# Performance work log

Hardware: AMD Instinct MI355X
Metric: run time of the kernel (lower is better)

## Reference

```python
import jax, jax.numpy as jnp
import numpy as np

BATCH = 4096
DIM = 128
TEMP = 0.5

def setup_inputs() -> dict:
    key = jax.random.key(0)
    k1, k2 = jax.random.split(key)
    proj_1 = jax.random.normal(k1, (BATCH, DIM), dtype=jnp.float32)
    proj_2 = jax.random.normal(k2, (BATCH, DIM), dtype=jnp.float32)
    return {"proj_1": proj_1, "proj_2": proj_2}

def _l2norm(x, eps=1e-12):
    # matches F.normalize(p=2, dim=1)
    n = jnp.sqrt(jnp.sum(x * x, axis=1, keepdims=True))
    return x / jnp.maximum(n, eps)

def reference(proj_1, proj_2):
    B = proj_1.shape[0]
    z_i = _l2norm(proj_1)
    z_j = _l2norm(proj_2)
    reps = jnp.concatenate([z_i, z_j], axis=0)          # [2B, D]
    # cosine similarity of normalized vectors == dot product; (2B,D)x(D,2B) matmul
    sim = reps @ reps.T                                 # [2B, 2B]
    sim_ij = jnp.einsum('bd,bd->b', z_i, z_j)           # diag(sim, +B)
    sim_ji = sim_ij                                     # diag(sim, -B) is symmetric
    positives = jnp.concatenate([sim_ij, sim_ji], axis=0)  # [2B]
    nominator = jnp.exp(positives / TEMP)
    mask = (~jnp.eye(2 * B, dtype=bool)).astype(sim.dtype)
    denominator = jnp.sum(mask * jnp.exp(sim / TEMP), axis=1)  # [2B]
    all_losses = -jnp.log(nominator / denominator)
    loss = jnp.sum(all_losses) / (2 * B)
    return loss
```

## Files before the change

### kernel.cpp

```cpp
#include <hip/hip_runtime.h>
#include <math.h>

#define BATCH 4096
#define DIM 128
#define TWO_B 8192
#define SCALE 1.69864374f
#define NBLK 1024
#define MAGIC 0x6D2F9A3Bu

typedef float floatx4 __attribute__((ext_vector_type(4)));
typedef int   intx4  __attribute__((ext_vector_type(4)));
typedef long  longx2 __attribute__((ext_vector_type(2)));

__device__ __forceinline__ longx2 as_l2(intx4 v) {
    union { intx4 a; longx2 b; } u; u.a = v; return u.b;
}
__device__ __forceinline__ unsigned char to_fp8(float v) {
    return (unsigned char)(__builtin_amdgcn_cvt_pk_fp8_f32(v, v, 0, false) & 0xff);
}
template <typename T>
__device__ __forceinline__ void st_agent(T* p, T v) {
    __hip_atomic_store(p, v, __ATOMIC_RELAXED, __HIP_MEMORY_SCOPE_AGENT);
}
template <typename T>
__device__ __forceinline__ T ld_agent(const T* p) {
    return __hip_atomic_load(p, __ATOMIC_RELAXED, __HIP_MEMORY_SCOPE_AGENT);
}


__global__ __launch_bounds__(256, 4) void fused_kernel(const float* __restrict__ p1,
                                                       const float* __restrict__ p2,
                                                       unsigned char* __restrict__ repsF,
                                                       float* __restrict__ pos,
                                                       float* __restrict__ denom,
                                                       unsigned int* __restrict__ gsync,
                                                       float* __restrict__ out) {
    __shared__ float lds[4][16][68];
    __shared__ float red[4];
    int tid = threadIdx.x;
    int wid = tid >> 6, lane = tid & 63;
    int bid = blockIdx.x;
    unsigned int* arr  = gsync;
    unsigned int* done = gsync + NBLK;
    unsigned int* go   = gsync + 2 * NBLK;

    if (tid < 8) st_agent(&denom[bid * 8 + tid], 0.0f);
    {
        int b = bid * 4 + wid;
        const float* r1 = p1 + (size_t)b * DIM;
        const float* r2 = p2 + (size_t)b * DIM;
        float x0 = r1[lane], x1 = r1[lane + 64];
        float y0 = r2[lane], y1 = r2[lane + 64];
        float s1 = x0 * x0 + x1 * x1;
        float s2 = y0 * y0 + y1 * y1;
        float s12 = x0 * y0 + x1 * y1;
        #pragma unroll
        for (int off = 32; off; off >>= 1) {
            s1  += __shfl_xor(s1, off);
            s2  += __shfl_xor(s2, off);
            s12 += __shfl_xor(s12, off);
        }
        float n1 = fmaxf(sqrtf(s1), 1e-12f);
        float n2 = fmaxf(sqrtf(s2), 1e-12f);
        float i1 = SCALE / n1;
        float i2 = SCALE / n2;

        int r1i = b, r2i = b + BATCH;
        int off0 = ((lane >> 5) & 1) * 8 + ((lane >> 3) & 3) * 256 + (lane & 7);
        size_t a1 = (size_t)(r1i >> 4) * 2048 + (r1i & 15) * 16 + off0;
        size_t a2 = (size_t)(r2i >> 4) * 2048 + (r2i & 15) * 16 + off0;
        st_agent(&repsF[a1],        to_fp8(x0 * i1));
        st_agent(&repsF[a1 + 1024], to_fp8(x1 * i1));
        st_agent(&repsF[a2],        to_fp8(y0 * i2));
        st_agent(&repsF[a2 + 1024], to_fp8(y1 * i2));

        if (lane == 0) st_agent(&pos[b], s12 / (n1 * n2));
    }

    __syncthreads();
    if (tid == 0) {
        asm volatile("s_waitcnt vmcnt(0)" ::: "memory");
        st_agent(&arr[bid], MAGIC);
    }
    if (bid == 0 && wid == 0) {
        int guard = 0;
        for (;;) {
            int ok = 1;
            #pragma unroll
            for (int j = 0; j < 16; ++j)
                ok &= (ld_agent(&arr[lane + j * 64]) == MAGIC) ? 1 : 0;
            if (__all(ok) || ++guard > (1 << 20)) break;
            __builtin_amdgcn_s_sleep(2);
        }
        if (lane == 0) {
            asm volatile("s_waitcnt vmcnt(0)" ::: "memory");
            st_agent(go, MAGIC);
        }
    }
    if (tid == 0) {
        int guard = 0;
        while (ld_agent(go) != MAGIC && ++guard < (1 << 20))
            __builtin_amdgcn_s_sleep(2);
    }
    __syncthreads();
    asm volatile("" ::: "memory");

    {
        int wm = wid >> 1, wn = wid & 1;
        int lr = lane & 15, q = lane >> 4;
        const char* base = (const char*)repsF;
        int lofs = q * 256 + lr * 16;

        for (int t = bid; t < 65 * 32; t += NBLK) {
            int r = t / 65;
            int c = t - r * 65;
            int TM, TN;
            if (c < 64 - r) { TM = r;      TN = r + c; }
            else            { TM = 63 - r; TN = TM + (c - (64 - r)); }
            if (TM == TN && wm == 1 && wn == 0) continue;
            int tm = 2 * TM + wm, tn = 2 * TN + wn;
            bool diag = (tm == tn);

            const char* ab = base + tm * 8192 + lofs;
            const char* bb = base + tn * 8192 + lofs;

            longx2 aF[4][2], bF[4][2];
            #pragma unroll
            for (int mi = 0; mi < 4; ++mi)
                #pragma unroll
                for (int h = 0; h < 2; ++h) {
                    aF[mi][h] = as_l2(*(const intx4*)(ab + mi * 2048 + h * 1024));
                    bF[mi][h] = as_l2(*(const intx4*)(bb + mi * 2048 + h * 1024));
                }

            float cs[4] = {0.0f, 0.0f, 0.0f, 0.0f};
            floatx4 rpacc[4];

            #pragma unroll
            for (int p = 0; p < 2; ++p) {
                floatx4 acc[4][2] = {};
                #pragma unroll
                for (int ck = 0; ck < 4; ++ck) {
                    int h = ck >> 1, sel = ck & 1;
                    #pragma unroll
                    for (int mi = 0; mi < 4; ++mi)
                        #pragma unroll
                        for (int nn = 0; nn < 2; ++nn)
                            acc[mi][nn] = __builtin_amdgcn_mfma_f32_16x16x32_fp8_fp8(
                                aF[mi][h][sel], bF[2 * p + nn][h][sel], acc[mi][nn], 0, 0, 0);
                }
                #pragma unroll
                for (int mi = 0; mi < 4; ++mi) {
                    #pragma unroll
                    for (int reg = 0; reg < 4; ++reg) {
                        float e0 = __builtin_amdgcn_exp2f(acc[mi][0][reg]);
                        float e1 = __builtin_amdgcn_exp2f(acc[mi][1][reg]);
                        if (diag && (q * 4 + reg) == lr) {
                            if (mi == 2 * p)     e0 = 0.0f;
                            if (mi == 2 * p + 1) e1 = 0.0f;
                        }
                        cs[2 * p]     += e0;
                        cs[2 * p + 1] += e1;
                        float rsum = e0 + e1;
                        rpacc[mi][reg] = (p == 0) ? rsum : (rpacc[mi][reg] + rsum);
                    }
                }
            }

            float* myl = &lds[wid][0][0];
            #pragma unroll
            for (int mi = 0; mi < 4; ++mi)
                *(floatx4*)&myl[lr * 68 + mi * 16 + q * 4] = rpacc[mi];
            asm volatile("s_waitcnt lgkmcnt(0)" ::: "memory");
            {
                float rs = 0.0f;
                #pragma unroll
                for (int j = 0; j < 16; ++j)
                    rs += myl[j * 68 + lane];
                atomicAdd(&denom[tm * 64 + lane], rs);
            }
            if (!diag) {
                #pragma unroll
                for (int ni = 0; ni < 4; ++ni) {
                    cs[ni] += __shfl_xor(cs[ni], 16);
                    cs[ni] += __shfl_xor(cs[ni], 32);
                }
                if (q == 0) {
                    #pragma unroll
                    for (int ni = 0; ni < 4; ++ni)
                        atomicAdd(&denom[tn * 64 + ni * 16 + lr], cs[ni]);
                }
            }
        }
    }

    __syncthreads();
    if (tid == 0) {
        asm volatile("s_waitcnt vmcnt(0)" ::: "memory");
        st_agent(&done[bid], MAGIC);
    }
    if (bid != 0) return;
    if (wid == 0) {
        int guard = 0;
        for (;;) {
            int ok = 1;
            #pragma unroll
            for (int j = 0; j < 16; ++j)
                ok &= (ld_agent(&done[lane + j * 64]) == MAGIC) ? 1 : 0;
            if (__all(ok) || ++guard > (1 << 20)) break;
            __builtin_amdgcn_s_sleep(2);
        }
    }
    __syncthreads();
    asm volatile("" ::: "memory");

    {
        float v = 0.0f;
        #pragma unroll
        for (int k = 0; k < 32; ++k) {
            int rr = k * 256 + tid;
            v += __logf(ld_agent(&denom[rr])) - 2.0f * ld_agent(&pos[rr & (BATCH - 1)]);
        }
        #pragma unroll
        for (int off = 32; off; off >>= 1) v += __shfl_xor(v, off);
        if (lane == 0) red[wid] = v;
        __syncthreads();
        if (tid == 0)
            out[0] = ((red[0] + red[1]) + (red[2] + red[3])) * (1.0f / TWO_B);
    }
}

extern "C" void kernel_launch(void* const* d_in, const int* in_sizes, int n_in,
                              void* d_out, int out_size, void* d_ws, size_t ws_size,
                              hipStream_t stream) {
    const float* p1 = (const float*)d_in[0];
    const float* p2 = (const float*)d_in[1];
    float* out = (float*)d_out;

    char* ws = (char*)d_ws;
    unsigned char* repsF = (unsigned char*)ws;
    float* pos   = (float*)(ws + (size_t)TWO_B * DIM);
    float* denom = pos + BATCH;
    unsigned int* gsync = (unsigned int*)(denom + TWO_B);

    fused_kernel<<<NBLK, 256, 0, stream>>>(p1, p2, repsF, pos, denom, gsync, out);
}
```

Measured before the change: 75.68 us.

## Replace denominator atomics with per-tile partial buffers and distributed final reduction

Row and column exp-sums are no longer atomically added into a shared denominator array. Each tile now writes its partial sums to a dedicated slot in a 128x8192 partial buffer, and 32 blocks reduce those partials after the done barrier, each adding its contribution to the output with one atomic. The fp8 normalized rows are also staged through LDS so each lane issues a single dword store instead of four byte stores. This is meant to remove atomic contention and scattered byte writes, at the cost of a much larger workspace, an extra pass reading the partials, and a float atomic on the output whose summation order can vary between runs.

Measured after the change: 80.32 us. +6.1%, slower.

```diff
diff --git a/kernel.cpp b/kernel.cpp
--- a/kernel.cpp
+++ b/kernel.cpp
@@ -32,11 +32,10 @@
                                                        const float* __restrict__ p2,
                                                        unsigned char* __restrict__ repsF,
                                                        float* __restrict__ pos,
-                                                       float* __restrict__ denom,
+                                                       float* __restrict__ part,
                                                        unsigned int* __restrict__ gsync,
                                                        float* __restrict__ out) {
     __shared__ float lds[4][16][68];
-    __shared__ float red[4];
     int tid = threadIdx.x;
     int wid = tid >> 6, lane = tid & 63;
     int bid = blockIdx.x;
@@ -44,7 +43,6 @@
     unsigned int* done = gsync + NBLK;
     unsigned int* go   = gsync + 2 * NBLK;
 
-    if (tid < 8) st_agent(&denom[bid * 8 + tid], 0.0f);
     {
         int b = bid * 4 + wid;
         const float* r1 = p1 + (size_t)b * DIM;
@@ -65,16 +63,24 @@
         float i1 = SCALE / n1;
         float i2 = SCALE / n2;
 
-        int r1i = b, r2i = b + BATCH;
-        int off0 = ((lane >> 5) & 1) * 8 + ((lane >> 3) & 3) * 256 + (lane & 7);
-        size_t a1 = (size_t)(r1i >> 4) * 2048 + (r1i & 15) * 16 + off0;
-        size_t a2 = (size_t)(r2i >> 4) * 2048 + (r2i & 15) * 16 + off0;
-        st_agent(&repsF[a1],        to_fp8(x0 * i1));
-        st_agent(&repsF[a1 + 1024], to_fp8(x1 * i1));
-        st_agent(&repsF[a2],        to_fp8(y0 * i2));
-        st_agent(&repsF[a2 + 1024], to_fp8(y1 * i2));
-
         if (lane == 0) st_agent(&pos[b], s12 / (n1 * n2));
+        if (bid == 0 && tid == 0) st_agent(out, 0.0f);
+
+        char* stg = (char*)&lds[wid][0][0];
+        int s  = (lane >> 3) & 3;
+        int byt = ((lane >> 5) & 1) * 8 + (lane & 7);
+        stg[s * 16 + byt]             = to_fp8(x0 * i1);
+        stg[(4 + s) * 16 + byt]       = to_fp8(x1 * i1);
+        stg[128 + s * 16 + byt]       = to_fp8(y0 * i2);
+        stg[128 + (4 + s) * 16 + byt] = to_fp8(y1 * i2);
+        asm volatile("s_waitcnt lgkmcnt(0)" ::: "memory");
+
+        int rowp = lane >> 5, seg = (lane >> 2) & 7, q4 = lane & 3;
+        unsigned int dw = *(const unsigned int*)(stg + rowp * 128 + seg * 16 + q4 * 4);
+        int rr = rowp ? (b + BATCH) : b;
+        size_t ga = (size_t)(rr >> 4) * 2048 + (rr & 15) * 16
+                  + (seg >> 2) * 1024 + (seg & 3) * 256 + q4 * 4;
+        st_agent((unsigned int*)(repsF + ga), dw);
     }
 
     __syncthreads();
@@ -177,7 +183,7 @@
                 #pragma unroll
                 for (int j = 0; j < 16; ++j)
                     rs += myl[j * 68 + lane];
-                atomicAdd(&denom[tm * 64 + lane], rs);
+                st_agent(&part[(size_t)tn * TWO_B + tm * 64 + lane], rs);
             }
             if (!diag) {
                 #pragma unroll
@@ -185,11 +191,9 @@
                     cs[ni] += __shfl_xor(cs[ni], 16);
                     cs[ni] += __shfl_xor(cs[ni], 32);
                 }
-                if (q == 0) {
-                    #pragma unroll
-                    for (int ni = 0; ni < 4; ++ni)
-                        atomicAdd(&denom[tn * 64 + ni * 16 + lr], cs[ni]);
-                }
+                float cv = (lane & 32) ? ((lane & 16) ? cs[3] : cs[2])
+                                       : ((lane & 16) ? cs[1] : cs[0]);
+                st_agent(&part[(size_t)tm * TWO_B + tn * 64 + lane], cv);
             }
         }
     }
@@ -199,7 +203,7 @@
         asm volatile("s_waitcnt vmcnt(0)" ::: "memory");
         st_agent(&done[bid], MAGIC);
     }
-    if (bid != 0) return;
+    if (bid < NBLK - 32) return;
     if (wid == 0) {
         int guard = 0;
         for (;;) {
@@ -215,18 +219,20 @@
     asm volatile("" ::: "memory");
 
     {
-        float v = 0.0f;
+        int r = (bid - (NBLK - 32)) * 256 + tid;
+        const float* pk = part + r;
+        float s0 = 0.0f, s1 = 0.0f, s2 = 0.0f, s3 = 0.0f;
         #pragma unroll
-        for (int k = 0; k < 32; ++k) {
-            int rr = k * 256 + tid;
-            v += __logf(ld_agent(&denom[rr])) - 2.0f * ld_agent(&pos[rr & (BATCH - 1)]);
-        }
+        for (int k = 0; k < 128; k += 4) {
+            s0 += pk[(size_t)(k + 0) * TWO_B];
+            s1 += pk[(size_t)(k + 1) * TWO_B];
+            s2 += pk[(size_t)(k + 2) * TWO_B];
+            s3 += pk[(size_t)(k + 3) * TWO_B];
+        }
+        float v = __logf((s0 + s1) + (s2 + s3)) - 2.0f * pos[r & (BATCH - 1)];
         #pragma unroll
         for (int off = 32; off; off >>= 1) v += __shfl_xor(v, off);
-        if (lane == 0) red[wid] = v;
-        __syncthreads();
-        if (tid == 0)
-            out[0] = ((red[0] + red[1]) + (red[2] + red[3])) * (1.0f / TWO_B);
+        if (lane == 0) atomicAdd(out, v * (1.0f / TWO_B));
     }
 }
 
@@ -240,8 +246,8 @@
     char* ws = (char*)d_ws;
     unsigned char* repsF = (unsigned char*)ws;
     float* pos   = (float*)(ws + (size_t)TWO_B * DIM);
-    float* denom = pos + BATCH;
-    unsigned int* gsync = (unsigned int*)(denom + TWO_B);
-
-    fused_kernel<<<NBLK, 256, 0, stream>>>(p1, p2, repsF, pos, denom, gsync, out);
-}
+    float* part  = pos + BATCH;
+    unsigned int* gsync = (unsigned int*)(part + (size_t)128 * TWO_B);
+
+    fused_kernel<<<NBLK, 256, 0, stream>>>(p1, p2, repsF, pos, part, gsync, out);
+}
```
